# Kernel tuning notes

Measured on AMD Instinct MI355X. Metric: run time of the kernel, lower is better.

The kernel has to match this reference:

```python
import jax, jax.numpy as jnp
import numpy as np

KNN_K = 5  # nearest neighbors for local density
PATCH_GRID = 14  # hard-coded p1=p2=14 in rearrange


def _tokens(x):
    # b c (p1 h) (p2 w) -> b (p1 p2) (h w c)
    B, C, H, W = x.shape
    P = PATCH_GRID
    h, w = H // P, W // P
    t = x.reshape(B, C, P, h, P, w).transpose(0, 2, 4, 3, 5, 1)
    return t.reshape(B, P * P, h * w * C)


def _forward(x, len_keep):
    t = _tokens(x)
    B, N, Cf = t.shape
    # pairwise Euclidean distance (torch.cdist) scaled by sqrt(C)
    sq = jnp.sum(t * t, axis=-1)  # [B, N]
    d2 = sq[:, :, None] + sq[:, None, :] - 2.0 * jnp.einsum('bnc,bmc->bnm', t, t)
    dist = jnp.sqrt(jnp.maximum(d2, 0.0)) / jnp.sqrt(jnp.asarray(Cf, dist_dtype := t.dtype))
    # k-NN local density
    neg_vals, _ = jax.lax.top_k(-dist, KNN_K)  # k smallest distances
    dist_nearest = -neg_vals  # [B, N, k]
    density = jnp.exp(-jnp.mean(dist_nearest ** 2, axis=-1))  # [B, N]
    kd = jax.random.fold_in(jax.random.key(1), 0)
    density = density + jax.random.uniform(kd, density.shape, dtype=density.dtype) * 1e-6
    # distance to nearest higher-density point (masked min reduction)
    maskf = (density[:, None, :] > density[:, :, None]).astype(dist.dtype)  # [B, N, N]
    dist_max = jnp.max(dist.reshape(B, -1), axis=-1)[:, None, None]
    dmin = jnp.min(dist * maskf + dist_max * (1.0 - maskf), axis=-1)  # [B, N]
    score = dmin * density
    # pick cluster centers: top len_keep scores
    _, index_down = jax.lax.top_k(score, len_keep)  # [B, K]
    # assign each token to nearest center
    dm_down = jnp.take_along_axis(dist, index_down[:, :, None], axis=1)  # [B, K, N]
    idx_cluster = jnp.argmin(dm_down, axis=1)  # [B, N]
    # force centers to their own cluster id
    idx_cluster = idx_cluster.at[jnp.arange(B)[:, None], index_down].set(
        jnp.arange(len_keep)[None, :])
    # per-cluster counts (every cluster id 0..K-1 present since centers self-assign)
    counts = jnp.sum(jax.nn.one_hot(idx_cluster, len_keep, dtype=jnp.int32), axis=1)  # [B, K]
    idx_counts = jnp.cumsum(counts, axis=-1)
    # pick one representative token per cluster via noisy sort
    kn = jax.random.fold_in(jax.random.key(1), 1)
    noise = jax.random.uniform(kn, (B, N), dtype=dist.dtype)
    order = jnp.argsort(idx_cluster.astype(dist.dtype) + noise, axis=-1)
    idx = jnp.take_along_axis(order, idx_counts - 1, axis=1)  # [B, K]
    return idx


def setup_inputs() -> dict:
    key = jax.random.key(0)
    x = jax.random.normal(key, (256, 3, 224, 224), dtype=jnp.float32)
    return {"x": x, "len_keep": 49}


def reference(x, len_keep):
    return _forward(x, len_keep)
```

## Files before the change

### kernel.cpp

```cpp
#include <hip/hip_runtime.h>
#include <stdint.h>

#define NTOK 196
#define KCL 49
#define IMG 224
#define IMG2 (224*224)
#define KB 64
#define LDP 68

typedef double f64x4 __attribute__((ext_vector_type(4)));

__host__ __device__ __forceinline__ void tf2x32(uint32_t k0, uint32_t k1,
    uint32_t x0, uint32_t x1, uint32_t* o0, uint32_t* o1) {
  uint32_t ks2 = k0 ^ k1 ^ 0x1BD11BDAu;
#define TFR(r) { x0 += x1; x1 = (x1 << r) | (x1 >> (32 - r)); x1 ^= x0; }
  x0 += k0; x1 += k1;
  TFR(13) TFR(15) TFR(26) TFR(6)
  x0 += k1; x1 += ks2 + 1u;
  TFR(17) TFR(29) TFR(16) TFR(24)
  x0 += ks2; x1 += k0 + 2u;
  TFR(13) TFR(15) TFR(26) TFR(6)
  x0 += k0; x1 += k1 + 3u;
  TFR(17) TFR(29) TFR(16) TFR(24)
  x0 += k1; x1 += ks2 + 4u;
  TFR(13) TFR(15) TFR(26) TFR(6)
  x0 += ks2; x1 += k0 + 5u;
#undef TFR
  *o0 = x0; *o1 = x1;
}

__device__ __forceinline__ float jax_uniform(uint32_t k0, uint32_t k1, uint32_t j) {
  uint32_t o0, o1;
  tf2x32(k0, k1, 0u, j, &o0, &o1);
  uint32_t bits = o0 ^ o1;
  return __uint_as_float((bits >> 9) | 0x3f800000u) - 1.0f;
}

__global__ void __launch_bounds__(256) k_diag(const float* __restrict__ x,
    double* __restrict__ sq, double* __restrict__ dist,
    unsigned long long* __restrict__ dmax) {
  int bid = blockIdx.x;
  int xcd = bid & 7;
  int s = bid >> 3;
  int b = xcd + 8 * (s / 7);
  int ti = s % 7;
  int n0b = ti * 32;
  int tid = threadIdx.x;

  __shared__ __align__(16) float As[32][LDP];
  __shared__ int rbN[32];
  __shared__ double prsh[3];
  __shared__ int okf;
  __shared__ double sqN[32];
  __shared__ double red2[256];

  if (tid < 32) {
    int n = n0b + tid; n = n < NTOK ? n : NTOK - 1;
    rbN[tid] = (n / 14) * 16 * IMG + (n % 14) * 16;
  }
  __syncthreads();

  const float* xb = x + (size_t)b * 3 * IMG2;
  int srow = tid >> 3;
  int sfo  = (tid & 7) * 8;
  int rN = rbN[srow];
  int lane = tid & 63;
  int wid  = tid >> 6;
  int wi = wid >> 1, wj = wid & 1;
  int aq = lane >> 4;
  const float* A0 = &As[0][0];
  int fragA = (wi * 16 + (lane & 15)) * LDP + aq;
  int fragB = (wj * 16 + (lane & 15)) * LDP + aq;

#define LOADD(d0,d1,kc) { int f0 = (kc) + sfo;                               \
    int c_ = f0 >> 8, h_ = (f0 >> 4) & 15, w_ = f0 & 15;                     \
    const float* p_ = xb + c_ * IMG2 + h_ * IMG + w_;                        \
    d0 = *(const float4*)(p_ + rN); d1 = *(const float4*)(p_ + rN + 4); }

  f64x4 acc = {0.0, 0.0, 0.0, 0.0};
  f64x4 acc0 = {0.0, 0.0, 0.0, 0.0};
  float4 ca0, ca1;
  LOADD(ca0, ca1, 0)

#pragma unroll
  for (int tt = 0; tt < 12; ++tt) {
    __syncthreads();
    *(float4*)&As[srow][sfo]     = ca0;
    *(float4*)&As[srow][sfo + 4] = ca1;
    __syncthreads();
    float4 na0, na1;
    if (tt < 11) LOADD(na0, na1, (tt + 1) * KB)
#pragma unroll
    for (int k = 0; k < KB; k += 4) {
      double av = (double)A0[fragA + k];
      double bv = (double)A0[fragB + k];
      acc = __builtin_amdgcn_mfma_f64_16x16x4f64(av, bv, acc, 0, 0, 0);
    }
    if (tt == 0) {
      if (wid == 0) {
        double q0 = (double)As[0][lane] * (double)As[0][lane];
        double q1 = (double)As[1][lane] * (double)As[0][lane];
        double q2 = (double)As[4][lane] * (double)As[0][lane];
#pragma unroll
        for (int off = 32; off; off >>= 1) {
          q0 += __shfl_down(q0, off);
          q1 += __shfl_down(q1, off);
          q2 += __shfl_down(q2, off);
        }
        if (lane == 0) { prsh[0] = q0; prsh[1] = q1; prsh[2] = q2; }
      }
      acc0 = acc;
    }
    ca0 = na0; ca1 = na1;
  }
#undef LOADD

  if (tid == 0) {
    double tol = 1e-9 * (1.0 + fabs(prsh[0]));
    int ok0  = fabs(prsh[0] - acc0[0]) <= tol;
    int okP1 = ok0 && (fabs(prsh[1] - acc0[1]) <= tol);
    int okP2 = ok0 && (fabs(prsh[2] - acc0[1]) <= tol);
    okf = okP1 ? 1 : (okP2 ? 2 : 0);
  }
  __syncthreads();
  int mode = okf;

  double (*Dt)[33] = (double(*)[33])A0;

  if (mode) {
#pragma unroll
    for (int i = 0; i < 4; ++i) {
      int lr = (mode == 1) ? (aq * 4 + i) : (aq + 4 * i);
      Dt[wi * 16 + lr][wj * 16 + (lane & 15)] = acc[i];
    }
  } else {
    double s00 = 0, s01 = 0, s10 = 0, s11 = 0;
    int ty2 = tid >> 4, tx2 = tid & 15;
    for (int kc = 0; kc < 768; kc += KB) {
      int f0 = kc + sfo;
      int c_ = f0 >> 8, h_ = (f0 >> 4) & 15, w_ = f0 & 15;
      const float* p_ = xb + c_ * IMG2 + h_ * IMG + w_;
      float4 la0 = *(const float4*)(p_ + rN), la1 = *(const float4*)(p_ + rN + 4);
      __syncthreads();
      *(float4*)&As[srow][sfo]     = la0;
      *(float4*)&As[srow][sfo + 4] = la1;
      __syncthreads();
      for (int j = 0; j < KB; ++j) {
        double a0 = (double)As[ty2][j], a1 = (double)As[ty2 + 16][j];
        double b0 = (double)As[tx2][j], b1 = (double)As[tx2 + 16][j];
        s00 += a0 * b0; s01 += a0 * b1; s10 += a1 * b0; s11 += a1 * b1;
      }
    }
    __syncthreads();
    Dt[ty2][tx2] = s00;       Dt[ty2][tx2 + 16] = s01;
    Dt[ty2 + 16][tx2] = s10;  Dt[ty2 + 16][tx2 + 16] = s11;
  }
  __syncthreads();

  if (tid < 32) {
    double v = Dt[tid][tid];
    sqN[tid] = v;
    int n = n0b + tid;
    if (n < NTOK) sq[b * NTOK + n] = v;
  }
  __syncthreads();

  const double SQ768 = sqrt(768.0);
  int lr2 = tid >> 3, lc0 = (tid & 7) * 4;
  double dv[4];
  double lmax = 0.0;
#pragma unroll
  for (int j = 0; j < 4; ++j) {
    double d2 = sqN[lr2] + sqN[lc0 + j] - 2.0 * Dt[lr2][lc0 + j];
    double d = sqrt(d2 > 0.0 ? d2 : 0.0) / SQ768;
    dv[j] = d;
    lmax = lmax > d ? lmax : d;
  }
  red2[tid] = lmax;
  __syncthreads();
  for (int st = 128; st; st >>= 1) {
    if (tid < st) { double o = red2[tid + st]; if (o > red2[tid]) red2[tid] = o; }
    __syncthreads();
  }
  if (tid == 0) atomicMax(&dmax[b], (unsigned long long)__double_as_longlong(red2[0]));

  double* Db = dist + (size_t)b * NTOK * NTOK;
  int n = n0b + lr2, m0 = n0b + lc0;
  if (n < NTOK && m0 < NTOK) {
    if (m0 + 3 < NTOK) {
      f64x4 v = {dv[0], dv[1], dv[2], dv[3]};
      *(f64x4*)(Db + (size_t)n * NTOK + m0) = v;
    } else {
#pragma unroll
      for (int j = 0; j < 4; ++j)
        if (m0 + j < NTOK) Db[(size_t)n * NTOK + m0 + j] = dv[j];
    }
  }
}

__global__ void __launch_bounds__(256) k_offdiag(const float* __restrict__ x,
    const double* __restrict__ sq, double* __restrict__ dist,
    unsigned long long* __restrict__ dmax) {
  int bid = blockIdx.x;
  int xcd = bid & 7;
  int s = bid >> 3;
  int b = xcd + 8 * (s / 21);
  int t = s % 21;
  int ti = 0, rem = t, rl = 6;
  while (rem >= rl) { rem -= rl; rl--; ti++; }
  int tj = ti + 1 + rem;
  int n0b = ti * 32, m0b = tj * 32;
  int tid = threadIdx.x;

  __shared__ __align__(16) float As[32][LDP];
  __shared__ __align__(16) float Bs[32][LDP];
  __shared__ int rbN[32], rbM[32];
  __shared__ double prsh[3];
  __shared__ int okf;

  if (tid < 32) {
    int n = n0b + tid; n = n < NTOK ? n : NTOK - 1;
    rbN[tid] = (n / 14) * 16 * IMG + (n % 14) * 16;
  } else if (tid < 64) {
    int m = m0b + (tid - 32); m = m < NTOK ? m : NTOK - 1;
    rbM[tid - 32] = (m / 14) * 16 * IMG + (m % 14) * 16;
  }
  __syncthreads();

  const float* xb = x + (size_t)b * 3 * IMG2;
  int srow = tid >> 3;
  int sfo  = (tid & 7) * 8;
  int rN = rbN[srow], rM = rbM[srow];
  int lane = tid & 63;
  int wid  = tid >> 6;
  int wi = wid >> 1, wj = wid & 1;
  int aq = lane >> 4;
  const float* Ap = &As[0][0];
  const float* Bp = &Bs[0][0];
  int fragA = (wi * 16 + (lane & 15)) * LDP + aq;
  int fragB = (wj * 16 + (lane & 15)) * LDP + aq;

#define LOADT(d0,d1,d2,d3,kc) { int f0 = (kc) + sfo;                         \
    int c_ = f0 >> 8, h_ = (f0 >> 4) & 15, w_ = f0 & 15;                     \
    const float* p_ = xb + c_ * IMG2 + h_ * IMG + w_;                        \
    d0 = *(const float4*)(p_ + rN); d1 = *(const float4*)(p_ + rN + 4);      \
    d2 = *(const float4*)(p_ + rM); d3 = *(const float4*)(p_ + rM + 4); }

  f64x4 acc = {0.0, 0.0, 0.0, 0.0};
  f64x4 acc0 = {0.0, 0.0, 0.0, 0.0};
  float4 ca0, ca1, cb0, cb1;
  LOADT(ca0, ca1, cb0, cb1, 0)

#pragma unroll
  for (int tt = 0; tt < 12; ++tt) {
    __syncthreads();
    *(float4*)&As[srow][sfo]     = ca0;
    *(float4*)&As[srow][sfo + 4] = ca1;
    *(float4*)&Bs[srow][sfo]     = cb0;
    *(float4*)&Bs[srow][sfo + 4] = cb1;
    __syncthreads();
    float4 na0, na1, nb0, nb1;
    if (tt < 11) LOADT(na0, na1, nb0, nb1, (tt + 1) * KB)
#pragma unroll
    for (int k = 0; k < KB; k += 4) {
      double av = (double)Ap[fragA + k];
      double bv = (double)Bp[fragB + k];
      acc = __builtin_amdgcn_mfma_f64_16x16x4f64(av, bv, acc, 0, 0, 0);
    }
    if (tt == 0) {
      if (wid == 0) {
        double q0 = (double)As[0][lane] * (double)Bs[0][lane];
        double q1 = (double)As[1][lane] * (double)Bs[0][lane];
        double q2 = (double)As[4][lane] * (double)Bs[0][lane];
#pragma unroll
        for (int off = 32; off; off >>= 1) {
          q0 += __shfl_down(q0, off);
          q1 += __shfl_down(q1, off);
          q2 += __shfl_down(q2, off);
        }
        if (lane == 0) { prsh[0] = q0; prsh[1] = q1; prsh[2] = q2; }
      }
      acc0 = acc;
    }
    ca0 = na0; ca1 = na1; cb0 = nb0; cb1 = nb1;
  }
#undef LOADT

  if (tid == 0) {
    double tol = 1e-9 * (1.0 + fabs(prsh[0]));
    int ok0  = fabs(prsh[0] - acc0[0]) <= tol;
    int okP1 = ok0 && (fabs(prsh[1] - acc0[1]) <= tol);
    int okP2 = ok0 && (fabs(prsh[2] - acc0[1]) <= tol);
    okf = okP1 ? 1 : (okP2 ? 2 : 0);
  }
  __syncthreads();
  int mode = okf;

  double (*Dt)[33] = (double(*)[33])Ap;

  if (mode) {
#pragma unroll
    for (int i = 0; i < 4; ++i) {
      int lr = (mode == 1) ? (aq * 4 + i) : (aq + 4 * i);
      Dt[wi * 16 + lr][wj * 16 + (lane & 15)] = acc[i];
    }
  } else {
    double s00 = 0, s01 = 0, s10 = 0, s11 = 0;
    int ty2 = tid >> 4, tx2 = tid & 15;
    for (int kc = 0; kc < 768; kc += KB) {
      int f0 = kc + sfo;
      int c_ = f0 >> 8, h_ = (f0 >> 4) & 15, w_ = f0 & 15;
      const float* p_ = xb + c_ * IMG2 + h_ * IMG + w_;
      float4 la0 = *(const float4*)(p_ + rN), la1 = *(const float4*)(p_ + rN + 4);
      float4 lb0 = *(const float4*)(p_ + rM), lb1 = *(const float4*)(p_ + rM + 4);
      __syncthreads();
      *(float4*)&As[srow][sfo]     = la0;
      *(float4*)&As[srow][sfo + 4] = la1;
      *(float4*)&Bs[srow][sfo]     = lb0;
      *(float4*)&Bs[srow][sfo + 4] = lb1;
      __syncthreads();
      for (int j = 0; j < KB; ++j) {
        double a0 = (double)As[ty2][j], a1 = (double)As[ty2 + 16][j];
        double b0 = (double)Bs[tx2][j], b1 = (double)Bs[tx2 + 16][j];
        s00 += a0 * b0; s01 += a0 * b1; s10 += a1 * b0; s11 += a1 * b1;
      }
    }
    __syncthreads();
    Dt[ty2][tx2] = s00;       Dt[ty2][tx2 + 16] = s01;
    Dt[ty2 + 16][tx2] = s10;  Dt[ty2 + 16][tx2 + 16] = s11;
  }
  __syncthreads();

  const double* sqb = sq + b * NTOK;
  const double SQ768 = sqrt(768.0);
  int lr2 = tid >> 3, lc0 = (tid & 7) * 4;
  double dv[4];
  double lmax = 0.0;
#pragma unroll
  for (int j = 0; j < 4; ++j) {
    int n = n0b + lr2, m = m0b + lc0 + j;
    int nn = n < NTOK ? n : NTOK - 1, mm = m < NTOK ? m : NTOK - 1;
    double d2 = sqb[nn] + sqb[mm] - 2.0 * Dt[lr2][lc0 + j];
    double d = sqrt(d2 > 0.0 ? d2 : 0.0) / SQ768;
    dv[j] = d;
    lmax = lmax > d ? lmax : d;
  }
#pragma unroll
  for (int j = 0; j < 4; ++j) Dt[lr2][lc0 + j] = dv[j];
  double* red = (double*)Bp;
  red[tid] = lmax;
  __syncthreads();
  for (int st = 128; st; st >>= 1) {
    if (tid < st) { double o = red[tid + st]; if (o > red[tid]) red[tid] = o; }
    __syncthreads();
  }
  if (tid == 0) atomicMax(&dmax[b], (unsigned long long)__double_as_longlong(red[0]));

  double* Db = dist + (size_t)b * NTOK * NTOK;
  {
    int n = n0b + lr2, m0 = m0b + lc0;
    if (n < NTOK && m0 < NTOK) {
      if (m0 + 3 < NTOK) {
        f64x4 v = {dv[0], dv[1], dv[2], dv[3]};
        *(f64x4*)(Db + (size_t)n * NTOK + m0) = v;
      } else {
#pragma unroll
        for (int j = 0; j < 4; ++j)
          if (m0 + j < NTOK) Db[(size_t)n * NTOK + m0 + j] = dv[j];
      }
    }
  }
  {
    int m = m0b + lr2, n0 = n0b + lc0;
    if (m < NTOK && n0 < NTOK) {
      if (n0 + 3 < NTOK) {
        f64x4 v = {Dt[lc0][lr2], Dt[lc0 + 1][lr2], Dt[lc0 + 2][lr2], Dt[lc0 + 3][lr2]};
        *(f64x4*)(Db + (size_t)m * NTOK + n0) = v;
      } else {
#pragma unroll
        for (int j = 0; j < 4; ++j)
          if (n0 + j < NTOK) Db[(size_t)m * NTOK + n0 + j] = Dt[lc0 + j][lr2];
      }
    }
  }
}

#define INS5(n0_,n1_,n2_,n3_,n4_,v_) {                                        \
  if ((v_) < n4_) { n4_ = (v_);                                               \
    if (n4_ < n3_) { double w_ = n3_; n3_ = n4_; n4_ = w_;                    \
      if (n3_ < n2_) { w_ = n2_; n2_ = n3_; n3_ = w_;                         \
        if (n2_ < n1_) { w_ = n1_; n1_ = n2_; n2_ = w_;                       \
          if (n1_ < n0_) { w_ = n0_; n0_ = n1_; n1_ = w_; } } } } } }

__device__ __forceinline__ void merge5(double a[5], const double b[5]) {
  double o[5];
  double ax = a[0], a1 = a[1], a2 = a[2], a3 = a[3], a4 = a[4];
  double bx = b[0], b1 = b[1], b2 = b[2], b3 = b[3], b4 = b[4];
#pragma unroll
  for (int p = 0; p < 5; ++p) {
    if (ax <= bx) { o[p] = ax; ax = a1; a1 = a2; a2 = a3; a3 = a4; a4 = 1e300; }
    else          { o[p] = bx; bx = b1; b1 = b2; b2 = b3; b3 = b4; b4 = 1e300; }
  }
#pragma unroll
  for (int p = 0; p < 5; ++p) a[p] = o[p];
}

__global__ void __launch_bounds__(1024) k_cluster4(const double* __restrict__ dist,
    const unsigned long long* __restrict__ dmax, int* __restrict__ out,
    uint32_t kd0, uint32_t kd1, uint32_t kn0, uint32_t kn1, int B) {
  int b = blockIdx.x;
  int tid = threadIdx.x;
  int lane = tid & 63, wid = tid >> 6;
  int t = tid & 255, q = tid >> 8;
  bool act = t < NTOK;
  int m0 = q * 49;
  const double* Db = dist + (size_t)b * NTOK * NTOK;
  __shared__ double nbsh[2][NTOK][5];
  __shared__ double dens[NTOK];
  __shared__ double score[NTOK];
  __shared__ int center[KCL];
  __shared__ short center_of[NTOK];
  __shared__ unsigned long long bkey[KCL];
  double dmaxv = __longlong_as_double((long long)dmax[b]);

  double nb[5] = {1e300, 1e300, 1e300, 1e300, 1e300};
  if (act) {
    const double* base = Db + t;
    for (int i = 0; i < 49; ++i) {
      double v = base[(size_t)(m0 + i) * NTOK];
      INS5(nb[0], nb[1], nb[2], nb[3], nb[4], v)
    }
    if (q == 1) {
#pragma unroll
      for (int p = 0; p < 5; ++p) nbsh[0][t][p] = nb[p];
    } else if (q == 3) {
#pragma unroll
      for (int p = 0; p < 5; ++p) nbsh[1][t][p] = nb[p];
    }
  }
  __syncthreads();
  if (act && q == 2) {
    double ob[5];
#pragma unroll
    for (int p = 0; p < 5; ++p) ob[p] = nbsh[1][t][p];
    merge5(nb, ob);
#pragma unroll
    for (int p = 0; p < 5; ++p) nbsh[1][t][p] = nb[p];
  }
  __syncthreads();
  if (tid < NTOK) {
    double ob[5];
#pragma unroll
    for (int p = 0; p < 5; ++p) ob[p] = nbsh[0][t][p];
    merge5(nb, ob);
#pragma unroll
    for (int p = 0; p < 5; ++p) ob[p] = nbsh[1][t][p];
    merge5(nb, ob);
    double acc = 0.0;
#pragma unroll
    for (int p = 0; p < 5; ++p) acc += nb[p] * nb[p];
    double d = exp(-(acc / 5.0));
    double u = (double)jax_uniform(kd0, kd1, (uint32_t)(b * NTOK + t));
    dens[t] = d + u * 1e-6;
  }
  __syncthreads();

  double vloc = dmaxv;
  if (act) {
    double dn = dens[t];
    const double* base = Db + t;
    for (int i = 0; i < 49; ++i) {
      double r = base[(size_t)(m0 + i) * NTOK];
      if (dens[m0 + i] > dn && r < vloc) vloc = r;
    }
  }
  __syncthreads();
  double* pm = &nbsh[0][0][0];
  if (act && q > 0) pm[(q - 1) * NTOK + t] = vloc;
  __syncthreads();
  if (tid < NTOK) {
    double v = vloc;
    double p1v = pm[t], p2v = pm[NTOK + t], p3v = pm[2 * NTOK + t];
    v = p1v < v ? p1v : v;
    v = p2v < v ? p2v : v;
    v = p3v < v ? p3v : v;
    score[t] = v * dens[t];
  }
  __syncthreads();

  if (wid == 0) {
    double s0 = (lane < NTOK) ? score[lane] : -1e300;
    double s1 = score[lane + 64];
    double s2 = score[lane + 128];
    double s3 = (lane + 192 < NTOK) ? score[lane + 192] : -1e300;
    for (int k = 0; k < KCL; ++k) {
      double mv = s0; int mi = lane;
      if (s1 > mv) { mv = s1; mi = lane + 64; }
      if (s2 > mv) { mv = s2; mi = lane + 128; }
      if (s3 > mv) { mv = s3; mi = lane + 192; }
#pragma unroll
      for (int off = 32; off; off >>= 1) {
        double ov = __shfl_down(mv, off); int oi = __shfl_down(mi, off);
        if (ov > mv || (ov == mv && oi < mi)) { mv = ov; mi = oi; }
      }
      mi = __shfl(mi, 0);
      if (lane == 0) center[k] = mi;
      if (mi == lane) s0 = -1e300;
      else if (mi == lane + 64) s1 = -1e300;
      else if (mi == lane + 128) s2 = -1e300;
      else if (mi == lane + 192) s3 = -1e300;
    }
  }
  __syncthreads();

  if (tid < NTOK) center_of[tid] = -1;
  __syncthreads();
  if (tid < KCL) { center_of[center[tid]] = (short)tid; bkey[tid] = 0ULL; }
  __syncthreads();
  int mycl = 0;
  if (tid < NTOK) {
    double best = 1e300; int bk = 0;
    for (int k = 0; k < KCL; ++k) {
      double d = Db[(size_t)center[k] * NTOK + tid];
      if (d < best) { best = d; bk = k; }
    }
    short co = center_of[tid];
    if (co >= 0) bk = co;
    mycl = bk;
  }
  __syncthreads();

  if (tid < NTOK) {
    float u = jax_uniform(kn0, kn1, (uint32_t)(b * NTOK + tid));
    float keyf = (float)mycl + u;
    unsigned long long key =
        ((unsigned long long)__float_as_uint(keyf) << 8) | (unsigned)tid;
    atomicMax(&bkey[mycl], key);
  }
  __syncthreads();
  if (tid < KCL) out[b * KCL + tid] = (int)(bkey[tid] & 0xFFu);
}

extern "C" void kernel_launch(void* const* d_in, const int* in_sizes, int n_in,
                              void* d_out, int out_size, void* d_ws, size_t ws_size,
                              hipStream_t stream) {
  const float* x = (const float*)d_in[0];
  int B = in_sizes[0] / (3 * IMG2);
  double* dist = (double*)d_ws;
  size_t distBytes = (size_t)B * NTOK * NTOK * sizeof(double);
  double* sq = (double*)((char*)d_ws + distBytes);
  unsigned long long* dmax =
      (unsigned long long*)((char*)sq + (size_t)B * NTOK * sizeof(double));
  int* out = (int*)d_out;

  uint32_t kd0, kd1, kn0, kn1;
  tf2x32(0u, 1u, 0u, 0u, &kd0, &kd1);
  tf2x32(0u, 1u, 0u, 1u, &kn0, &kn1);

  hipMemsetAsync(dmax, 0, B * sizeof(unsigned long long), stream);
  k_diag<<<dim3(8 * 32 * 7), dim3(256), 0, stream>>>(x, sq, dist, dmax);
  k_offdiag<<<dim3(8 * 32 * 21), dim3(256), 0, stream>>>(x, sq, dist, dmax);
  k_cluster4<<<dim3(B), dim3(1024), 0, stream>>>(dist, dmax, out, kd0, kd1, kn0, kn1, B);
}
```

Measured before the change: 293.6 us.

## Split K across waves in off-diagonal Gram tile and reduce via LDS

The off-diagonal distance kernel previously had each of four waves compute one 16x16 output quadrant over the full K range. Now each wave computes the full 32x32 tile (four MFMA accumulators) over a quarter of each K chunk, and the partial sums are combined through a two-step LDS reduction. The layout-probe check now accumulates its dot products across all K chunks and compares them against the reduced full-K result. This reduces redundant LDS fragment loads and raises MFMA independence per wave, at the cost of more accumulator registers and extra barriers and LDS traffic in the reduction.

Measured after the change: 301.8 us. +2.8%, slower.

```diff
diff --git a/kernel.cpp b/kernel.cpp
--- a/kernel.cpp
+++ b/kernel.cpp
@@ -6,6 +6,7 @@
 #define IMG 224
 #define IMG2 (224*224)
 #define KB 64
+#define NKT 12
 #define LDP 68
 
 typedef double f64x4 __attribute__((ext_vector_type(4)));
@@ -83,13 +84,13 @@
   LOADD(ca0, ca1, 0)
 
 #pragma unroll
-  for (int tt = 0; tt < 12; ++tt) {
+  for (int tt = 0; tt < NKT; ++tt) {
     __syncthreads();
     *(float4*)&As[srow][sfo]     = ca0;
     *(float4*)&As[srow][sfo + 4] = ca1;
     __syncthreads();
     float4 na0, na1;
-    if (tt < 11) LOADD(na0, na1, (tt + 1) * KB)
+    if (tt < NKT - 1) LOADD(na0, na1, (tt + 1) * KB)
 #pragma unroll
     for (int k = 0; k < KB; k += 4) {
       double av = (double)A0[fragA + k];
@@ -215,7 +216,6 @@
   __shared__ __align__(16) float As[32][LDP];
   __shared__ __align__(16) float Bs[32][LDP];
   __shared__ int rbN[32], rbM[32];
-  __shared__ double prsh[3];
   __shared__ int okf;
 
   if (tid < 32) {
@@ -233,12 +233,15 @@
   int rN = rbN[srow], rM = rbM[srow];
   int lane = tid & 63;
   int wid  = tid >> 6;
-  int wi = wid >> 1, wj = wid & 1;
+  int lr16 = lane & 15;
   int aq = lane >> 4;
+  int kb0 = wid * 16;
   const float* Ap = &As[0][0];
   const float* Bp = &Bs[0][0];
-  int fragA = (wi * 16 + (lane & 15)) * LDP + aq;
-  int fragB = (wj * 16 + (lane & 15)) * LDP + aq;
+  int fa0 = lr16 * LDP + kb0 + aq;
+  int fa1 = (16 + lr16) * LDP + kb0 + aq;
+  int fb0 = fa0;
+  int fb1 = fa1;
 
 #define LOADT(d0,d1,d2,d3,kc) { int f0 = (kc) + sfo;                         \
     int c_ = f0 >> 8, h_ = (f0 >> 4) & 15, w_ = f0 & 15;                     \
@@ -246,13 +249,13 @@
     d0 = *(const float4*)(p_ + rN); d1 = *(const float4*)(p_ + rN + 4);      \
     d2 = *(const float4*)(p_ + rM); d3 = *(const float4*)(p_ + rM + 4); }
 
-  f64x4 acc = {0.0, 0.0, 0.0, 0.0};
-  f64x4 acc0 = {0.0, 0.0, 0.0, 0.0};
+  f64x4 acc00 = {0,0,0,0}, acc01 = {0,0,0,0}, acc10 = {0,0,0,0}, acc11 = {0,0,0,0};
+  double q0 = 0.0, q1 = 0.0, q2 = 0.0;
   float4 ca0, ca1, cb0, cb1;
   LOADT(ca0, ca1, cb0, cb1, 0)
 
 #pragma unroll
-  for (int tt = 0; tt < 12; ++tt) {
+  for (int tt = 0; tt < NKT; ++tt) {
     __syncthreads();
     *(float4*)&As[srow][sfo]     = ca0;
     *(float4*)&As[srow][sfo + 4] = ca1;
@@ -260,49 +263,92 @@
     *(float4*)&Bs[srow][sfo + 4] = cb1;
     __syncthreads();
     float4 na0, na1, nb0, nb1;
-    if (tt < 11) LOADT(na0, na1, nb0, nb1, (tt + 1) * KB)
-#pragma unroll
-    for (int k = 0; k < KB; k += 4) {
-      double av = (double)Ap[fragA + k];
-      double bv = (double)Bp[fragB + k];
-      acc = __builtin_amdgcn_mfma_f64_16x16x4f64(av, bv, acc, 0, 0, 0);
-    }
-    if (tt == 0) {
-      if (wid == 0) {
-        double q0 = (double)As[0][lane] * (double)Bs[0][lane];
-        double q1 = (double)As[1][lane] * (double)Bs[0][lane];
-        double q2 = (double)As[4][lane] * (double)Bs[0][lane];
-#pragma unroll
-        for (int off = 32; off; off >>= 1) {
-          q0 += __shfl_down(q0, off);
-          q1 += __shfl_down(q1, off);
-          q2 += __shfl_down(q2, off);
-        }
-        if (lane == 0) { prsh[0] = q0; prsh[1] = q1; prsh[2] = q2; }
+    if (tt < NKT - 1) LOADT(na0, na1, nb0, nb1, (tt + 1) * KB)
+#pragma unroll
+    for (int ss = 0; ss < 4; ++ss) {
+      int o = ss * 4;
+      double a0 = (double)Ap[fa0 + o];
+      double a1 = (double)Ap[fa1 + o];
+      double b0 = (double)Bp[fb0 + o];
+      double b1 = (double)Bp[fb1 + o];
+      acc00 = __builtin_amdgcn_mfma_f64_16x16x4f64(a0, b0, acc00, 0, 0, 0);
+      acc01 = __builtin_amdgcn_mfma_f64_16x16x4f64(a0, b1, acc01, 0, 0, 0);
+      acc10 = __builtin_amdgcn_mfma_f64_16x16x4f64(a1, b0, acc10, 0, 0, 0);
+      acc11 = __builtin_amdgcn_mfma_f64_16x16x4f64(a1, b1, acc11, 0, 0, 0);
+    }
+    if (wid == 0) {
+      double bl = (double)Bs[0][lane];
+      q0 += (double)As[0][lane] * bl;
+      q1 += (double)As[1][lane] * bl;
+      q2 += (double)As[4][lane] * bl;
+    }
+    ca0 = na0; ca1 = na1; cb0 = nb0; cb1 = nb1;
+  }
+#undef LOADT
+
+  double* R0 = (double*)&Bs[0][0];
+  double* R1 = (double*)&As[0][0];
+  __syncthreads();
+#define STORE_ACC(R) {                                                        \
+    R[(0*4+0)*64+lane]=acc00[0]; R[(0*4+1)*64+lane]=acc00[1];                 \
+    R[(0*4+2)*64+lane]=acc00[2]; R[(0*4+3)*64+lane]=acc00[3];                 \
+    R[(1*4+0)*64+lane]=acc01[0]; R[(1*4+1)*64+lane]=acc01[1];                 \
+    R[(1*4+2)*64+lane]=acc01[2]; R[(1*4+3)*64+lane]=acc01[3];                 \
+    R[(2*4+0)*64+lane]=acc10[0]; R[(2*4+1)*64+lane]=acc10[1];                 \
+    R[(2*4+2)*64+lane]=acc10[2]; R[(2*4+3)*64+lane]=acc10[3];                 \
+    R[(3*4+0)*64+lane]=acc11[0]; R[(3*4+1)*64+lane]=acc11[1];                 \
+    R[(3*4+2)*64+lane]=acc11[2]; R[(3*4+3)*64+lane]=acc11[3]; }
+#define ADD_ACC(R) {                                                          \
+    acc00[0]+=R[(0*4+0)*64+lane]; acc00[1]+=R[(0*4+1)*64+lane];               \
+    acc00[2]+=R[(0*4+2)*64+lane]; acc00[3]+=R[(0*4+3)*64+lane];               \
+    acc01[0]+=R[(1*4+0)*64+lane]; acc01[1]+=R[(1*4+1)*64+lane];               \
+    acc01[2]+=R[(1*4+2)*64+lane]; acc01[3]+=R[(1*4+3)*64+lane];               \
+    acc10[0]+=R[(2*4+0)*64+lane]; acc10[1]+=R[(2*4+1)*64+lane];               \
+    acc10[2]+=R[(2*4+2)*64+lane]; acc10[3]+=R[(2*4+3)*64+lane];               \
+    acc11[0]+=R[(3*4+0)*64+lane]; acc11[1]+=R[(3*4+1)*64+lane];               \
+    acc11[2]+=R[(3*4+2)*64+lane]; acc11[3]+=R[(3*4+3)*64+lane]; }
+  if (wid == 2) STORE_ACC(R0)
+  else if (wid == 3) STORE_ACC(R1)
+  __syncthreads();
+  if (wid == 0) ADD_ACC(R0)
+  else if (wid == 1) ADD_ACC(R1)
+  __syncthreads();
+  if (wid == 1) STORE_ACC(R0)
+  __syncthreads();
+  if (wid == 0) ADD_ACC(R0)
+#undef STORE_ACC
+#undef ADD_ACC
+
+  if (wid == 0) {
+#pragma unroll
+    for (int off = 32; off; off >>= 1) {
+      q0 += __shfl_down(q0, off);
+      q1 += __shfl_down(q1, off);
+      q2 += __shfl_down(q2, off);
+    }
+    if (lane == 0) {
+      double tol = 1e-9 * (1.0 + fabs(q0));
+      int ok0  = fabs(q0 - acc00[0]) <= tol;
+      int okP1 = ok0 && (fabs(q1 - acc00[1]) <= tol);
+      int okP2 = ok0 && (fabs(q2 - acc00[1]) <= tol);
+      okf = okP1 ? 1 : (okP2 ? 2 : 0);
+    }
+  }
+  __syncthreads();
+  int mode = okf;
+
+  double (*Dt)[33] = (double(*)[33])(&As[0][0]);
+
+  if (mode) {
+    if (wid == 0) {
+#pragma unroll
+      for (int i = 0; i < 4; ++i) {
+        int lr = (mode == 1) ? (aq * 4 + i) : (aq + 4 * i);
+        Dt[lr][lr16]           = acc00[i];
+        Dt[lr][16 + lr16]      = acc01[i];
+        Dt[16 + lr][lr16]      = acc10[i];
+        Dt[16 + lr][16 + lr16] = acc11[i];
       }
-      acc0 = acc;
-    }
-    ca0 = na0; ca1 = na1; cb0 = nb0; cb1 = nb1;
-  }
-#undef LOADT
-
-  if (tid == 0) {
-    double tol = 1e-9 * (1.0 + fabs(prsh[0]));
-    int ok0  = fabs(prsh[0] - acc0[0]) <= tol;
-    int okP1 = ok0 && (fabs(prsh[1] - acc0[1]) <= tol);
-    int okP2 = ok0 && (fabs(prsh[2] - acc0[1]) <= tol);
-    okf = okP1 ? 1 : (okP2 ? 2 : 0);
-  }
-  __syncthreads();
-  int mode = okf;
-
-  double (*Dt)[33] = (double(*)[33])Ap;
-
-  if (mode) {
-#pragma unroll
-    for (int i = 0; i < 4; ++i) {
-      int lr = (mode == 1) ? (aq * 4 + i) : (aq + 4 * i);
-      Dt[wi * 16 + lr][wj * 16 + (lane & 15)] = acc[i];
     }
   } else {
     double s00 = 0, s01 = 0, s10 = 0, s11 = 0;
@@ -347,7 +393,7 @@
   }
 #pragma unroll
   for (int j = 0; j < 4; ++j) Dt[lr2][lc0 + j] = dv[j];
-  double* red = (double*)Bp;
+  double* red = (double*)&Bs[0][0];
   red[tid] = lmax;
   __syncthreads();
   for (int st = 128; st; st >>= 1) {
```
